# Kernel optimization log

Hardware: AMD Instinct MI355X
Metric: run time of the kernel (lower is better)

Reference implementation:

```python
import jax, jax.numpy as jnp
import numpy as np


def setup_inputs() -> dict:
    key = jax.random.key(0)
    k1, k2 = jax.random.split(key)
    pred = jax.random.normal(k1, (8, 4096, 2), dtype=jnp.float32)
    target = jax.random.normal(k2, (8, 4096, 2), dtype=jnp.float32)
    return {"pred": pred, "target": target}


def reference(pred, target):
    # pred: [B, N, D], target: [B, M, D]
    # pairwise euclidean distances per batch: [B, N, M]
    diff = pred[:, :, None, :] - target[:, None, :, :]  # [B, N, M, D]
    dist = jnp.sqrt(jnp.sum(diff * diff, axis=-1))       # [B, N, M]
    # directed Hausdorff h(a,b) = max_i min_j d(a_i, b_j)
    h_ab = jnp.max(jnp.min(dist, axis=2), axis=1)        # [B]
    h_ba = jnp.max(jnp.min(dist, axis=1), axis=1)        # [B]
    score = jnp.maximum(h_ab, h_ba)                      # symmetric Hausdorff per batch
    return jnp.mean(score)
```

## Files before the change

### kernel.cpp

```cpp
#include <hip/hip_runtime.h>
#include <hip/hip_bf16.h>
#include <math.h>


#define B 8
#define N 4096
#define TPB 256
#define IB 8
#define JC 32
#define JTILE (N / JC)
#define ITILES (N / TPB)

__global__ __launch_bounds__(TPB) void hk_partial(const float* __restrict__ pred,
                                                  const float* __restrict__ target,
                                                  float* __restrict__ pw) {
    const int bx  = blockIdx.x;
    const int ib  = bx & 1;
    const int jc  = bx >> 1;
    const int b   = blockIdx.y;
    const int dir = blockIdx.z;

    const float2* __restrict__ P =
        reinterpret_cast<const float2*>(dir == 0 ? pred : target) + (size_t)b * N;
    const float*  __restrict__ Qf =
        (dir == 0 ? target : pred) + (size_t)b * N * 2 + (size_t)jc * JTILE * 2;

    __shared__ float4 sQ[JTILE / 2];
    if (threadIdx.x < JTILE / 2)
        sQ[threadIdx.x] = reinterpret_cast<const float4*>(Qf)[threadIdx.x];
    __syncthreads();

    float m2x[IB], m2y[IB], pp[IB], mn[IB];
    const int i0 = ib * (TPB * IB) + threadIdx.x;
    #pragma unroll
    for (int k = 0; k < IB; ++k) {
        float2 p = P[i0 + k * TPB];
        m2x[k] = -2.f * p.x;
        m2y[k] = -2.f * p.y;
        pp[k]  = fmaf(p.x, p.x, p.y * p.y);
        mn[k]  = 3.402823466e38f;
    }

    #pragma unroll 4
    for (int j = 0; j < JTILE / 2; ++j) {
        float4 q = sQ[j];
        float qqa = fmaf(q.x, q.x, q.y * q.y);
        float qqb = fmaf(q.z, q.z, q.w * q.w);
        #pragma unroll
        for (int k = 0; k < IB; ++k) {
            float ta = fmaf(m2x[k], q.x, fmaf(m2y[k], q.y, qqa));
            float tb = fmaf(m2x[k], q.z, fmaf(m2y[k], q.w, qqb));
            mn[k] = fminf(mn[k], fminf(ta, tb));
        }
    }

    float* dst = pw + (size_t)((dir * B + b) * JC + jc) * N;
    #pragma unroll
    for (int k = 0; k < IB; ++k)
        dst[i0 + k * TPB] = mn[k] + pp[k];
}

__global__ __launch_bounds__(TPB) void hk_maxred(const float* __restrict__ pw,
                                                 float* __restrict__ pw2) {
    const int tile = blockIdx.x;
    const int b    = blockIdx.y;
    const int dir  = blockIdx.z;
    const int t    = threadIdx.x;

    const float* base = pw + (size_t)((dir * B + b) * JC) * N + tile * TPB + t;
    float mnv = base[0];
    #pragma unroll
    for (int jc = 1; jc < JC; ++jc) mnv = fminf(mnv, base[(size_t)jc * N]);

    float mx = mnv;
    #pragma unroll
    for (int off = 32; off > 0; off >>= 1)
        mx = fmaxf(mx, __shfl_down(mx, off, 64));

    __shared__ float sred[TPB / 64];
    if ((t & 63) == 0) sred[t >> 6] = mx;
    __syncthreads();
    if (t == 0) {
        float bm = sred[0];
        #pragma unroll
        for (int w = 1; w < TPB / 64; ++w) bm = fmaxf(bm, sred[w]);
        pw2[(dir * B + b) * ITILES + tile] = bm;
    }
}

__global__ __launch_bounds__(64) void hk_final(const float* __restrict__ pw2,
                                               float* __restrict__ out) {
    const int t = threadIdx.x;
    __shared__ float h2[2 * B];
    if (t < 2 * B) {
        float mx = pw2[t * ITILES];
        #pragma unroll
        for (int k = 1; k < ITILES; ++k) mx = fmaxf(mx, pw2[t * ITILES + k]);
        h2[t] = mx;
    }
    __syncthreads();
    if (t == 0) {
        float s = 0.f;
        #pragma unroll
        for (int b = 0; b < B; ++b)
            s += sqrtf(fmaxf(fmaxf(h2[b], h2[B + b]), 0.f));
        out[0] = s * (1.0f / B);
    }
}

extern "C" void kernel_launch(void* const* d_in, const int* in_sizes, int n_in,
                              void* d_out, int out_size, void* d_ws, size_t ws_size,
                              hipStream_t stream) {
    const float* pred   = (const float*)d_in[0];
    const float* target = (const float*)d_in[1];
    float* out = (float*)d_out;
    float* pw  = (float*)d_ws;
    float* pw2 = (float*)((char*)d_ws + (size_t)2 * B * JC * N * sizeof(float));

    dim3 g1(64, B, 2);
    hk_partial<<<g1, TPB, 0, stream>>>(pred, target, pw);
    dim3 g2(ITILES, B, 2);
    hk_maxred<<<g2, TPB, 0, stream>>>(pw, pw2);
    hk_final<<<1, 64, 0, stream>>>(pw2, out);
}
```

Before: 76.98 us.

## Fuse three kernels into one using last-block atomic counters for reductions

New measurement: 191.1 us. 2.48x slower.

```diff
diff --git a/kernel.cpp b/kernel.cpp
--- a/kernel.cpp
+++ b/kernel.cpp
@@ -9,29 +9,39 @@
 #define IB 8
 #define JC 32
 #define JTILE (N / JC)
-#define ITILES (N / TPB)
+#define NGROUP 32
+#define BPG 32
 
-__global__ __launch_bounds__(TPB) void hk_partial(const float* __restrict__ pred,
-                                                  const float* __restrict__ target,
-                                                  float* __restrict__ pw) {
+__global__ __launch_bounds__(TPB) void hk_main(const float* __restrict__ pred,
+                                               const float* __restrict__ target,
+                                               int* __restrict__ cnt,
+                                               int* __restrict__ cnt2,
+                                               int* __restrict__ slots,
+                                               float* __restrict__ pw,
+                                               float* __restrict__ out) {
     const int bx  = blockIdx.x;
     const int ib  = bx & 1;
     const int jc  = bx >> 1;
     const int b   = blockIdx.y;
     const int dir = blockIdx.z;
+    const int t   = threadIdx.x;
+
+    __shared__ float4 sQ[JTILE / 2];
+    __shared__ float  sred[TPB / 64];
+    __shared__ float  sh2[2 * B];
+    __shared__ int    sflag, sflag2;
 
     const float2* __restrict__ P =
         reinterpret_cast<const float2*>(dir == 0 ? pred : target) + (size_t)b * N;
     const float*  __restrict__ Qf =
         (dir == 0 ? target : pred) + (size_t)b * N * 2 + (size_t)jc * JTILE * 2;
 
-    __shared__ float4 sQ[JTILE / 2];
-    if (threadIdx.x < JTILE / 2)
-        sQ[threadIdx.x] = reinterpret_cast<const float4*>(Qf)[threadIdx.x];
+    if (t < JTILE / 2)
+        sQ[t] = reinterpret_cast<const float4*>(Qf)[t];
     __syncthreads();
 
     float m2x[IB], m2y[IB], pp[IB], mn[IB];
-    const int i0 = ib * (TPB * IB) + threadIdx.x;
+    const int i0 = ib * (TPB * IB) + t;
     #pragma unroll
     for (int k = 0; k < IB; ++k) {
         float2 p = P[i0 + k * TPB];
@@ -58,52 +68,54 @@
     #pragma unroll
     for (int k = 0; k < IB; ++k)
         dst[i0 + k * TPB] = mn[k] + pp[k];
-}
 
-__global__ __launch_bounds__(TPB) void hk_maxred(const float* __restrict__ pw,
-                                                 float* __restrict__ pw2) {
-    const int tile = blockIdx.x;
-    const int b    = blockIdx.y;
-    const int dir  = blockIdx.z;
-    const int t    = threadIdx.x;
+    __threadfence();
+    if (t == 0) {
+        int old = atomicAdd(&cnt[(dir * B + b) * 2 + ib], 1);
+        sflag = (old == BPG - 1);
+    }
+    __syncthreads();
+    if (!sflag) return;
+    __threadfence();
 
-    const float* base = pw + (size_t)((dir * B + b) * JC) * N + tile * TPB + t;
-    float mnv = base[0];
+    const float* base = pw + (size_t)((dir * B + b) * JC) * N;
+    float mx = -3.402823466e38f;
     #pragma unroll
-    for (int jc = 1; jc < JC; ++jc) mnv = fminf(mnv, base[(size_t)jc * N]);
-
-    float mx = mnv;
+    for (int k = 0; k < IB; ++k) {
+        const int i = ib * (TPB * IB) + t + k * TPB;
+        float mnv = base[i];
+        #pragma unroll
+        for (int j2 = 1; j2 < JC; ++j2)
+            mnv = fminf(mnv, base[(size_t)j2 * N + i]);
+        mx = fmaxf(mx, mnv);
+    }
     #pragma unroll
     for (int off = 32; off > 0; off >>= 1)
         mx = fmaxf(mx, __shfl_down(mx, off, 64));
-
-    __shared__ float sred[TPB / 64];
     if ((t & 63) == 0) sred[t >> 6] = mx;
     __syncthreads();
+
     if (t == 0) {
         float bm = sred[0];
         #pragma unroll
         for (int w = 1; w < TPB / 64; ++w) bm = fmaxf(bm, sred[w]);
-        pw2[(dir * B + b) * ITILES + tile] = bm;
+        atomicMax(&slots[dir * B + b], __float_as_int(bm));
+        __threadfence();
+        int old2 = atomicAdd(cnt2, 1);
+        sflag2 = (old2 == NGROUP - 1);
     }
-}
+    __syncthreads();
+    if (!sflag2) return;
+    __threadfence();
 
-__global__ __launch_bounds__(64) void hk_final(const float* __restrict__ pw2,
-                                               float* __restrict__ out) {
-    const int t = threadIdx.x;
-    __shared__ float h2[2 * B];
-    if (t < 2 * B) {
-        float mx = pw2[t * ITILES];
-        #pragma unroll
-        for (int k = 1; k < ITILES; ++k) mx = fmaxf(mx, pw2[t * ITILES + k]);
-        h2[t] = mx;
-    }
+    if (t < 2 * B)
+        sh2[t] = __int_as_float(atomicMax(&slots[t], 0));
     __syncthreads();
     if (t == 0) {
         float s = 0.f;
         #pragma unroll
-        for (int b = 0; b < B; ++b)
-            s += sqrtf(fmaxf(fmaxf(h2[b], h2[B + b]), 0.f));
+        for (int bb = 0; bb < B; ++bb)
+            s += sqrtf(fmaxf(fmaxf(sh2[bb], sh2[B + bb]), 0.f));
         out[0] = s * (1.0f / B);
     }
 }
@@ -114,12 +126,14 @@
     const float* pred   = (const float*)d_in[0];
     const float* target = (const float*)d_in[1];
     float* out = (float*)d_out;
-    float* pw  = (float*)d_ws;
-    float* pw2 = (float*)((char*)d_ws + (size_t)2 * B * JC * N * sizeof(float));
+
+    int*   cnt   = (int*)d_ws;
+    int*   cnt2  = (int*)d_ws + 32;
+    int*   slots = (int*)d_ws + 64;
+    float* pw    = (float*)((char*)d_ws + 1024);
+
+    hipMemsetAsync(d_ws, 0, 1024, stream);
 
     dim3 g1(64, B, 2);
-    hk_partial<<<g1, TPB, 0, stream>>>(pred, target, pw);
-    dim3 g2(ITILES, B, 2);
-    hk_maxred<<<g2, TPB, 0, stream>>>(pw, pw2);
-    hk_final<<<1, 64, 0, stream>>>(pw2, out);
+    hk_main<<<g1, TPB, 0, stream>>>(pred, target, cnt, cnt2, slots, pw, out);
 }
```
